# Kernel tuning notes

Measured on AMD Instinct MI355X. Metric: run time of the kernel, lower is better.

Reference implementation:

```python
import jax, jax.numpy as jnp
import numpy as np

N_EMB = 1024
HEAD_SIZE = 64
BLOCK_SIZE = 2048
B, T = 8, 2048


def setup_inputs() -> dict:
    key = jax.random.key(0)
    kx, kq, kk, kv = jax.random.split(key, 4)
    scale = 1.0 / (N_EMB ** 0.5)
    x = jax.random.normal(kx, (B, T, N_EMB), dtype=jnp.float32)
    Wq = jax.random.uniform(kq, (N_EMB, HEAD_SIZE), dtype=jnp.float32) * scale
    Wk = jax.random.uniform(kk, (N_EMB, HEAD_SIZE), dtype=jnp.float32) * scale
    Wv = jax.random.uniform(kv, (N_EMB, HEAD_SIZE), dtype=jnp.float32) * scale
    return {"x": x, "Wq": Wq, "Wk": Wk, "Wv": Wv}


def reference(x, Wq, Wk, Wv):
    # Faithful to Head.__call__ with is_training=False.
    # NOTE: original code applies NO 1/sqrt(head_size) scaling to the scores.
    Bt, Tt, _ = x.shape
    q = x @ Wq                      # (B, T, H)
    k = x @ Wk                      # (B, T, H)
    v = x @ Wv                      # (B, T, H)
    wei = jnp.einsum('bth,bsh->bts', q, k)  # (B, T, T)
    causal = jnp.tril(jnp.ones((Tt, Tt), dtype=bool))
    wei = jnp.where(causal, wei, -jnp.inf)
    wei = jax.nn.softmax(wei, axis=-1)
    out = jnp.einsum('bts,bsh->bth', wei, v)  # (B, T, H)
    return out
```

## Files before the change

### kernel.cpp

```cpp
#include <hip/hip_runtime.h>
#include <hip/hip_bf16.h>

#define BB 8
#define TT 2048
#define EE 1024
#define HH 64

typedef __attribute__((ext_vector_type(8))) short short8;
typedef __attribute__((ext_vector_type(4))) float f32x4;

__device__ inline f32x4 mfma_16x16x32(short8 a, short8 b, f32x4 c) {
  return __builtin_amdgcn_mfma_f32_16x16x32_bf16(a, b, c, 0, 0, 0);
}

__device__ inline void gload_lds16(const __hip_bfloat16* g, __hip_bfloat16* l) {
  __builtin_amdgcn_global_load_lds((const __attribute__((address_space(1))) void*)g,
                                   (__attribute__((address_space(3))) void*)l,
                                   16, 0, 0);
}

__device__ inline short f2bf(float f) {
  __hip_bfloat16 h = __float2bfloat16(f);
  return *reinterpret_cast<short*>(&h);
}
__device__ inline float bf2f(short s) {
  __hip_bfloat16 h = *reinterpret_cast<__hip_bfloat16*>(&s);
  return __bfloat162float(h);
}

__global__ void prep_w(const float* __restrict__ Wq, const float* __restrict__ Wk,
                       const float* __restrict__ Wv,
                       __hip_bfloat16* __restrict__ Wthi,
                       __hip_bfloat16* __restrict__ Wtlo) {
  const int n = blockIdx.x;
  const int m = n >> 6;
  const int h = n & 63;
  const float* W = (m == 0) ? Wq : (m == 1) ? Wk : Wv;
  const int e0 = threadIdx.x * 4;
#pragma unroll
  for (int j = 0; j < 4; ++j) {
    const float w = W[(e0 + j) * 64 + h];
    const __hip_bfloat16 hi = __float2bfloat16(w);
    Wthi[n * 1024 + e0 + j] = hi;
    Wtlo[n * 1024 + e0 + j] = __float2bfloat16(w - __bfloat162float(hi));
  }
}

__global__ __launch_bounds__(256) void qkv_gemm(
    const float* __restrict__ x,
    const __hip_bfloat16* __restrict__ Wthi, const __hip_bfloat16* __restrict__ Wtlo,
    __hip_bfloat16* __restrict__ qhi, __hip_bfloat16* __restrict__ qlo,
    __hip_bfloat16* __restrict__ khi, __hip_bfloat16* __restrict__ klo,
    __hip_bfloat16* __restrict__ vT) {
  __shared__ __hip_bfloat16 Ahi[2][64 * 72];
  __shared__ __hip_bfloat16 Alo[2][64 * 72];
  __shared__ __hip_bfloat16 Bhi[2][192 * 64];
  __shared__ __hip_bfloat16 Blo[2][128 * 64];

  const int tid  = threadIdx.x;
  const int wave = tid >> 6;
  const int lane = tid & 63;
  const int row0 = blockIdx.x * 64;

  const int lr = tid >> 2;
  const int le = (tid & 3) * 16;
  const float* xrow = x + (row0 + lr) * 1024 + le;

  f32x4 acc[12];
#pragma unroll
  for (int j = 0; j < 12; ++j) acc[j] = f32x4{0.f, 0.f, 0.f, 0.f};

  const int l15 = lane & 15, l4 = lane >> 4;

  auto issue_B = [&](int c, int buf) {
    const int g = (lane & 7) ^ ((lane >> 3) & 7);
#pragma unroll
    for (int s = 0; s < 6; ++s) {
      const int qq = wave * 6 + s;
      const int n  = qq * 8 + (lane >> 3);
      gload_lds16(Wthi + n * 1024 + c * 64 + g * 8, &Bhi[buf][qq * 512]);
      if (qq < 16)
        gload_lds16(Wtlo + n * 1024 + c * 64 + g * 8, &Blo[buf][qq * 512]);
    }
  };
  auto write_A = [&](int buf, const f32x4* xr) {
    short8 h0, h1, l0, l1;
    const float* xf = (const float*)xr;
#pragma unroll
    for (int j = 0; j < 8; ++j) {
      const float v = xf[j];
      const short h = f2bf(v);
      h0[j] = h;
      l0[j] = f2bf(v - bf2f(h));
    }
#pragma unroll
    for (int j = 0; j < 8; ++j) {
      const float v = xf[8 + j];
      const short h = f2bf(v);
      h1[j] = h;
      l1[j] = f2bf(v - bf2f(h));
    }
    *(short8*)&Ahi[buf][lr * 72 + le]     = h0;
    *(short8*)&Ahi[buf][lr * 72 + le + 8] = h1;
    *(short8*)&Alo[buf][lr * 72 + le]     = l0;
    *(short8*)&Alo[buf][lr * 72 + le + 8] = l1;
  };
  auto compute = [&](int buf) {
    const int tr = wave * 16 + l15;
    short8 ah0 = *(const short8*)&Ahi[buf][tr * 72 + l4 * 8];
    short8 ah1 = *(const short8*)&Ahi[buf][tr * 72 + 32 + l4 * 8];
    short8 al0 = *(const short8*)&Alo[buf][tr * 72 + l4 * 8];
    short8 al1 = *(const short8*)&Alo[buf][tr * 72 + 32 + l4 * 8];
#pragma unroll
    for (int j = 0; j < 12; ++j) {
      const int n  = j * 16 + l15;
      const int o0 = ((l4)     ^ (n & 7)) * 8;
      const int o1 = ((4 + l4) ^ (n & 7)) * 8;
      short8 bh0 = *(const short8*)&Bhi[buf][n * 64 + o0];
      short8 bh1 = *(const short8*)&Bhi[buf][n * 64 + o1];
      acc[j] = mfma_16x16x32(ah0, bh0, acc[j]);
      acc[j] = mfma_16x16x32(ah1, bh1, acc[j]);
      if (j < 8) {
        short8 bl0 = *(const short8*)&Blo[buf][n * 64 + o0];
        short8 bl1 = *(const short8*)&Blo[buf][n * 64 + o1];
        acc[j] = mfma_16x16x32(ah0, bl0, acc[j]);
        acc[j] = mfma_16x16x32(ah1, bl1, acc[j]);
        acc[j] = mfma_16x16x32(al0, bh0, acc[j]);
        acc[j] = mfma_16x16x32(al1, bh1, acc[j]);
      }
    }
  };

  f32x4 xr[4], xn[4];
  {
    const f32x4* p = (const f32x4*)xrow;
    xr[0] = p[0]; xr[1] = p[1]; xr[2] = p[2]; xr[3] = p[3];
  }
  issue_B(0, 0);
  __builtin_amdgcn_s_waitcnt(0);
  write_A(0, xr);
  __syncthreads();

  for (int c = 0; c < 16; ++c) {
    const int p = c & 1;
    if (c < 15) {
      const f32x4* pp = (const f32x4*)(xrow + (c + 1) * 64);
      xn[0] = pp[0]; xn[1] = pp[1]; xn[2] = pp[2]; xn[3] = pp[3];
      issue_B(c + 1, p ^ 1);
    }
    compute(p);
    if (c < 15) {
      __builtin_amdgcn_s_waitcnt(0);
      write_A(p ^ 1, xn);
    }
    __syncthreads();
  }

  const int strip = wave * 16;
#pragma unroll
  for (int j = 0; j < 12; ++j) {
    const int n  = j * 16 + l15;
    const int mm = n >> 6;
    const int h  = n & 63;
#pragma unroll
    for (int r = 0; r < 4; ++r) {
      const int trow = row0 + strip + l4 * 4 + r;
      const float val = acc[j][r];
      const __hip_bfloat16 hi = __float2bfloat16(val);
      const __hip_bfloat16 lo = __float2bfloat16(val - __bfloat162float(hi));
      if (mm == 0) {
        qhi[trow * 64 + h] = hi;
        qlo[trow * 64 + h] = lo;
      } else if (mm == 1) {
        khi[trow * 64 + h] = hi;
        klo[trow * 64 + h] = lo;
      } else {
        const int bb = trow >> 11, tl = trow & 2047;
        vT[(bb * 64 + h) * 2048 + tl] = hi;
      }
    }
  }
}

__global__ __launch_bounds__(256, 1) void attn(
    const __hip_bfloat16* __restrict__ qhi, const __hip_bfloat16* __restrict__ qlo,
    const __hip_bfloat16* __restrict__ khi, const __hip_bfloat16* __restrict__ klo,
    const __hip_bfloat16* __restrict__ vT, float* __restrict__ out) {
  __shared__ __hip_bfloat16 Psm[4][64 * 72];
  __shared__ float Osm[4][64][65];
  __shared__ float Msm[4][64];
  __shared__ float Lsm[4][64];

  const int tid   = threadIdx.x;
  const int wave  = tid >> 6;
  const int lane  = tid & 63;
  const int bid   = blockIdx.x;
  const int b     = bid & 7;
  const int strip = 31 - (bid >> 3);
  const int t0    = strip * 64;
  const int l15 = lane & 15, l4 = lane >> 4;

  const int kt_total = strip + 1;
  const int chunk    = (kt_total + 3) >> 2;
  const int ktb      = wave * chunk;
  const int kte      = min(ktb + chunk, kt_total);

  short8 qh0[4], qh1[4], ql0[4], ql1[4];
#pragma unroll
  for (int m = 0; m < 4; ++m) {
    const __hip_bfloat16* qph = qhi + (b * 2048 + t0 + m * 16 + l15) * 64;
    const __hip_bfloat16* qpl = qlo + (b * 2048 + t0 + m * 16 + l15) * 64;
    qh0[m] = *(const short8*)(qph + l4 * 8);
    qh1[m] = *(const short8*)(qph + 32 + l4 * 8);
    ql0[m] = *(const short8*)(qpl + l4 * 8);
    ql1[m] = *(const short8*)(qpl + 32 + l4 * 8);
  }

  f32x4 acc[4][4];
#pragma unroll
  for (int m = 0; m < 4; ++m)
#pragma unroll
    for (int j = 0; j < 4; ++j) acc[m][j] = f32x4{0.f, 0.f, 0.f, 0.f};
  float m_[4][4], l_[4][4];
#pragma unroll
  for (int m = 0; m < 4; ++m)
#pragma unroll
    for (int r = 0; r < 4; ++r) { m_[m][r] = -1e30f; l_[m][r] = 0.f; }

  const __hip_bfloat16* kbase_h = khi + (size_t)b * 2048 * 64;
  const __hip_bfloat16* kbase_l = klo + (size_t)b * 2048 * 64;
  const __hip_bfloat16* vbase   = vT + (size_t)b * 64 * 2048;

  for (int kt = ktb; kt < kte; ++kt) {
    const int k0 = kt << 6;
    const bool diag = (k0 == t0);

    short8 kh0[4], kh1[4], kl0[4], kl1[4];
#pragma unroll
    for (int j = 0; j < 4; ++j) {
      const __hip_bfloat16* kph = kbase_h + (k0 + j * 16 + l15) * 64;
      const __hip_bfloat16* kpl = kbase_l + (k0 + j * 16 + l15) * 64;
      kh0[j] = *(const short8*)(kph + l4 * 8);
      kh1[j] = *(const short8*)(kph + 32 + l4 * 8);
      kl0[j] = *(const short8*)(kpl + l4 * 8);
      kl1[j] = *(const short8*)(kpl + 32 + l4 * 8);
    }

#pragma unroll
    for (int m = 0; m < 4; ++m) {
      f32x4 s[4];
#pragma unroll
      for (int j = 0; j < 4; ++j) {
        if (diag && j > m) {
          s[j] = f32x4{-1e30f, -1e30f, -1e30f, -1e30f};
          continue;
        }
        f32x4 z = f32x4{0.f, 0.f, 0.f, 0.f};
        z = mfma_16x16x32(qh0[m], kh0[j], z);
        z = mfma_16x16x32(qh1[m], kh1[j], z);
        z = mfma_16x16x32(qh0[m], kl0[j], z);
        z = mfma_16x16x32(qh1[m], kl1[j], z);
        z = mfma_16x16x32(ql0[m], kh0[j], z);
        z = mfma_16x16x32(ql1[m], kh1[j], z);
        s[j] = z;
      }
      if (diag) {
#pragma unroll
        for (int j = 0; j < 4; ++j) {
          if (j != m) continue;
          const int key = j * 16 + l15;
#pragma unroll
          for (int r = 0; r < 4; ++r) {
            const int row = m * 16 + l4 * 4 + r;
            if (key > row) s[j][r] = -1e30f;
          }
        }
      }

      float mx[4], rs[4], al[4];
#pragma unroll
      for (int r = 0; r < 4; ++r)
        mx[r] = fmaxf(fmaxf(s[0][r], s[1][r]), fmaxf(s[2][r], s[3][r]));
      for (int off = 1; off < 16; off <<= 1) {
#pragma unroll
        for (int r = 0; r < 4; ++r) mx[r] = fmaxf(mx[r], __shfl_xor(mx[r], off));
      }
#pragma unroll
      for (int r = 0; r < 4; ++r) {
        const float mn = fmaxf(m_[m][r], mx[r]);
        al[r] = __expf(m_[m][r] - mn);
        m_[m][r] = mn;
        rs[r] = 0.f;
      }
#pragma unroll
      for (int j = 0; j < 4; ++j) {
#pragma unroll
        for (int r = 0; r < 4; ++r) {
          const float pv = __expf(s[j][r] - m_[m][r]);
          s[j][r] = pv;
          rs[r] += pv;
        }
      }
      for (int off = 1; off < 16; off <<= 1) {
#pragma unroll
        for (int r = 0; r < 4; ++r) rs[r] += __shfl_xor(rs[r], off);
      }
#pragma unroll
      for (int r = 0; r < 4; ++r) l_[m][r] = l_[m][r] * al[r] + rs[r];
#pragma unroll
      for (int j = 0; j < 4; ++j)
#pragma unroll
        for (int r = 0; r < 4; ++r) acc[m][j][r] *= al[r];

#pragma unroll
      for (int j = 0; j < 4; ++j)
#pragma unroll
        for (int r = 0; r < 4; ++r)
          Psm[wave][(m * 16 + l4 * 4 + r) * 72 + j * 16 + l15] =
              __float2bfloat16(s[j][r]);
    }

    short8 vf0[4], vf1[4];
#pragma unroll
    for (int j = 0; j < 4; ++j) {
      const __hip_bfloat16* vp = vbase + (j * 16 + l15) * 2048 + k0;
      vf0[j] = *(const short8*)(vp + l4 * 8);
      vf1[j] = *(const short8*)(vp + 32 + l4 * 8);
    }

    __builtin_amdgcn_s_waitcnt(0);

#pragma unroll
    for (int m = 0; m < 4; ++m) {
      short8 pf0 = *(const short8*)&Psm[wave][(m * 16 + l15) * 72 + l4 * 8];
      short8 pf1 = *(const short8*)&Psm[wave][(m * 16 + l15) * 72 + 32 + l4 * 8];
#pragma unroll
      for (int j = 0; j < 4; ++j) {
        acc[m][j] = mfma_16x16x32(pf0, vf0[j], acc[m][j]);
        acc[m][j] = mfma_16x16x32(pf1, vf1[j], acc[m][j]);
      }
    }
  }

#pragma unroll
  for (int m = 0; m < 4; ++m) {
#pragma unroll
    for (int j = 0; j < 4; ++j)
#pragma unroll
      for (int r = 0; r < 4; ++r)
        Osm[wave][m * 16 + l4 * 4 + r][j * 16 + l15] = acc[m][j][r];
    if (l15 == 0) {
#pragma unroll
      for (int r = 0; r < 4; ++r) {
        Msm[wave][m * 16 + l4 * 4 + r] = m_[m][r];
        Lsm[wave][m * 16 + l4 * 4 + r] = l_[m][r];
      }
    }
  }
  __syncthreads();

#pragma unroll
  for (int rr = 0; rr < 16; ++rr) {
    const int row = wave * 16 + rr;
    float M = fmaxf(fmaxf(Msm[0][row], Msm[1][row]),
                    fmaxf(Msm[2][row], Msm[3][row]));
    float L = 0.f, O = 0.f;
#pragma unroll
    for (int w = 0; w < 4; ++w) {
      const float a = __expf(Msm[w][row] - M);
      L += Lsm[w][row] * a;
      O += Osm[w][row][lane] * a;
    }
    out[(b * 2048 + t0 + row) * 64 + lane] = O / L;
  }
}

extern "C" void kernel_launch(void* const* d_in, const int* in_sizes, int n_in,
                              void* d_out, int out_size, void* d_ws, size_t ws_size,
                              hipStream_t stream) {
  const float* x  = (const float*)d_in[0];
  const float* Wq = (const float*)d_in[1];
  const float* Wk = (const float*)d_in[2];
  const float* Wv = (const float*)d_in[3];
  float* out = (float*)d_out;

  char* ws = (char*)d_ws;
  __hip_bfloat16* Wthi = (__hip_bfloat16*)ws;
  __hip_bfloat16* Wtlo = (__hip_bfloat16*)(ws + 393216);
  __hip_bfloat16* qhi  = (__hip_bfloat16*)(ws + 786432);
  __hip_bfloat16* qlo  = (__hip_bfloat16*)(ws + 786432 + 1 * 2097152);
  __hip_bfloat16* khi  = (__hip_bfloat16*)(ws + 786432 + 2 * 2097152);
  __hip_bfloat16* klo  = (__hip_bfloat16*)(ws + 786432 + 3 * 2097152);
  __hip_bfloat16* vT   = (__hip_bfloat16*)(ws + 786432 + 4 * 2097152);

  prep_w<<<192, 256, 0, stream>>>(Wq, Wk, Wv, Wthi, Wtlo);
  qkv_gemm<<<256, 256, 0, stream>>>(x, Wthi, Wtlo, qhi, qlo, khi, klo, vT);
  attn<<<256, 256, 0, stream>>>(qhi, qlo, khi, klo, vT, out);
}
```

Before: 172.2 us.

## Split causal attention into per-wave KV chunks with separate merge kernel

Replaces the one-block-per-strip attention kernel with a split-KV scheme. Each wave independently owns a (batch, strip, chunk) work item of up to 8 chunks, giving 1824 waves in 456 blocks at occupancy 2, and writes a normalized bf16 partial output plus max and sum to workspace. A new merge kernel combines the partials per strip. This targets the load imbalance and low occupancy of the triangular causal workload, at the cost of an extra launch, global round-trips for the partials, and bf16 rounding of partial outputs. It also narrows the waitcnt so only LDS counters are waited on.

```diff
diff --git a/kernel.cpp b/kernel.cpp
--- a/kernel.cpp
+++ b/kernel.cpp
@@ -27,6 +27,8 @@
   __hip_bfloat16 h = *reinterpret_cast<__hip_bfloat16*>(&s);
   return __bfloat162float(h);
 }
+
+#define WAIT_LGKM0() __builtin_amdgcn_s_waitcnt(0xC07F)
 
 __global__ void prep_w(const float* __restrict__ Wq, const float* __restrict__ Wk,
                        const float* __restrict__ Wv,
@@ -182,28 +184,39 @@
   }
 }
 
-__global__ __launch_bounds__(256, 1) void attn(
+__global__ __launch_bounds__(256, 2) void attn_part(
     const __hip_bfloat16* __restrict__ qhi, const __hip_bfloat16* __restrict__ qlo,
     const __hip_bfloat16* __restrict__ khi, const __hip_bfloat16* __restrict__ klo,
-    const __hip_bfloat16* __restrict__ vT, float* __restrict__ out) {
+    const __hip_bfloat16* __restrict__ vT,
+    __hip_bfloat16* __restrict__ partO, float* __restrict__ partM,
+    float* __restrict__ partL) {
   __shared__ __hip_bfloat16 Psm[4][64 * 72];
-  __shared__ float Osm[4][64][65];
-  __shared__ float Msm[4][64];
-  __shared__ float Lsm[4][64];
-
-  const int tid   = threadIdx.x;
-  const int wave  = tid >> 6;
-  const int lane  = tid & 63;
-  const int bid   = blockIdx.x;
-  const int b     = bid & 7;
-  const int strip = 31 - (bid >> 3);
-  const int t0    = strip * 64;
+
+  const int tid  = threadIdx.x;
+  const int wave = tid >> 6;
+  const int lane = tid & 63;
   const int l15 = lane & 15, l4 = lane >> 4;
 
-  const int kt_total = strip + 1;
-  const int chunk    = (kt_total + 3) >> 2;
-  const int ktb      = wave * chunk;
-  const int kte      = min(ktb + chunk, kt_total);
+  const int w = 1823 - (blockIdx.x * 4 + wave);
+  const int b = w / 228;
+  int v = w % 228;
+  int s, ci;
+  if (v < 28) {
+    s = 0;
+    while (v >= s + 1) { v -= s + 1; ++s; }
+    ci = v;
+  } else {
+    const int g = v - 28;
+    s = 7 + (g >> 3);
+    ci = g & 7;
+  }
+  const int ntile = s + 1;
+  const int nch   = (ntile < 8) ? ntile : 8;
+  const int base  = ntile / nch, rem = ntile % nch;
+  const int tb    = ci * base + ((ci < rem) ? ci : rem);
+  const int tcnt  = base + ((ci < rem) ? 1 : 0);
+  const int t0    = s * 64;
+  const int pidx  = (b * 32 + s) * 8 + ci;
 
   short8 qh0[4], qh1[4], ql0[4], ql1[4];
 #pragma unroll
@@ -231,9 +244,10 @@
   const __hip_bfloat16* kbase_l = klo + (size_t)b * 2048 * 64;
   const __hip_bfloat16* vbase   = vT + (size_t)b * 64 * 2048;
 
-  for (int kt = ktb; kt < kte; ++kt) {
+  for (int tt = 0; tt < tcnt; ++tt) {
+    const int kt = tb + tt;
     const int k0 = kt << 6;
-    const bool diag = (k0 == t0);
+    const bool diag = (kt == s);
 
     short8 kh0[4], kh1[4], kl0[4], kl1[4];
 #pragma unroll
@@ -248,11 +262,11 @@
 
 #pragma unroll
     for (int m = 0; m < 4; ++m) {
-      f32x4 s[4];
+      f32x4 s_[4];
 #pragma unroll
       for (int j = 0; j < 4; ++j) {
         if (diag && j > m) {
-          s[j] = f32x4{-1e30f, -1e30f, -1e30f, -1e30f};
+          s_[j] = f32x4{-1e30f, -1e30f, -1e30f, -1e30f};
           continue;
         }
         f32x4 z = f32x4{0.f, 0.f, 0.f, 0.f};
@@ -262,25 +276,21 @@
         z = mfma_16x16x32(qh1[m], kl1[j], z);
         z = mfma_16x16x32(ql0[m], kh0[j], z);
         z = mfma_16x16x32(ql1[m], kh1[j], z);
-        s[j] = z;
+        s_[j] = z;
       }
       if (diag) {
-#pragma unroll
-        for (int j = 0; j < 4; ++j) {
-          if (j != m) continue;
-          const int key = j * 16 + l15;
-#pragma unroll
-          for (int r = 0; r < 4; ++r) {
-            const int row = m * 16 + l4 * 4 + r;
-            if (key > row) s[j][r] = -1e30f;
-          }
+        const int key = m * 16 + l15;
+#pragma unroll
+        for (int r = 0; r < 4; ++r) {
+          const int row = m * 16 + l4 * 4 + r;
+          if (key > row) s_[m][r] = -1e30f;
         }
       }
 
       float mx[4], rs[4], al[4];
 #pragma unroll
       for (int r = 0; r < 4; ++r)
-        mx[r] = fmaxf(fmaxf(s[0][r], s[1][r]), fmaxf(s[2][r], s[3][r]));
+        mx[r] = fmaxf(fmaxf(s_[0][r], s_[1][r]), fmaxf(s_[2][r], s_[3][r]));
       for (int off = 1; off < 16; off <<= 1) {
 #pragma unroll
         for (int r = 0; r < 4; ++r) mx[r] = fmaxf(mx[r], __shfl_xor(mx[r], off));
@@ -296,8 +306,8 @@
       for (int j = 0; j < 4; ++j) {
 #pragma unroll
         for (int r = 0; r < 4; ++r) {
-          const float pv = __expf(s[j][r] - m_[m][r]);
-          s[j][r] = pv;
+          const float pv = __expf(s_[j][r] - m_[m][r]);
+          s_[j][r] = pv;
           rs[r] += pv;
         }
       }
@@ -317,7 +327,7 @@
 #pragma unroll
         for (int r = 0; r < 4; ++r)
           Psm[wave][(m * 16 + l4 * 4 + r) * 72 + j * 16 + l15] =
-              __float2bfloat16(s[j][r]);
+              __float2bfloat16(s_[j][r]);
     }
 
     short8 vf0[4], vf1[4];
@@ -328,7 +338,7 @@
       vf1[j] = *(const short8*)(vp + 32 + l4 * 8);
     }
 
-    __builtin_amdgcn_s_waitcnt(0);
+    WAIT_LGKM0();
 
 #pragma unroll
     for (int m = 0; m < 4; ++m) {
@@ -344,34 +354,49 @@
 
 #pragma unroll
   for (int m = 0; m < 4; ++m) {
+    float inv[4];
+#pragma unroll
+    for (int r = 0; r < 4; ++r) inv[r] = (l_[m][r] > 0.f) ? 1.f / l_[m][r] : 0.f;
 #pragma unroll
     for (int j = 0; j < 4; ++j)
 #pragma unroll
       for (int r = 0; r < 4; ++r)
-        Osm[wave][m * 16 + l4 * 4 + r][j * 16 + l15] = acc[m][j][r];
+        partO[(size_t)pidx * 4096 + (m * 16 + l4 * 4 + r) * 64 + j * 16 + l15] =
+            __float2bfloat16(acc[m][j][r] * inv[r]);
     if (l15 == 0) {
 #pragma unroll
       for (int r = 0; r < 4; ++r) {
-        Msm[wave][m * 16 + l4 * 4 + r] = m_[m][r];
-        Lsm[wave][m * 16 + l4 * 4 + r] = l_[m][r];
-      }
-    }
-  }
-  __syncthreads();
-
-#pragma unroll
+        partM[pidx * 64 + m * 16 + l4 * 4 + r] = m_[m][r];
+        partL[pidx * 64 + m * 16 + l4 * 4 + r] = l_[m][r];
+      }
+    }
+  }
+}
+
+__global__ __launch_bounds__(256) void attn_merge(
+    const __hip_bfloat16* __restrict__ partO, const float* __restrict__ partM,
+    const float* __restrict__ partL, float* __restrict__ out) {
+  const int bs = blockIdx.x;
+  const int b = bs >> 5, s = bs & 31;
+  const int nch = (s + 1 < 8) ? (s + 1) : 8;
+  const int tid = threadIdx.x;
+  const int h = tid & 63, rg = tid >> 6;
+
+#pragma unroll 4
   for (int rr = 0; rr < 16; ++rr) {
-    const int row = wave * 16 + rr;
-    float M = fmaxf(fmaxf(Msm[0][row], Msm[1][row]),
-                    fmaxf(Msm[2][row], Msm[3][row]));
+    const int row = rg * 16 + rr;
+    float M = -1e30f;
+    for (int c = 0; c < nch; ++c)
+      M = fmaxf(M, partM[(bs * 8 + c) * 64 + row]);
     float L = 0.f, O = 0.f;
-#pragma unroll
-    for (int w = 0; w < 4; ++w) {
-      const float a = __expf(Msm[w][row] - M);
-      L += Lsm[w][row] * a;
-      O += Osm[w][row][lane] * a;
-    }
-    out[(b * 2048 + t0 + row) * 64 + lane] = O / L;
+    for (int c = 0; c < nch; ++c) {
+      const float a = __expf(partM[(bs * 8 + c) * 64 + row] - M) *
+                      partL[(bs * 8 + c) * 64 + row];
+      L += a;
+      O += a * __bfloat162float(
+               partO[(size_t)(bs * 8 + c) * 4096 + row * 64 + h]);
+    }
+    out[(b * 2048 + s * 64 + row) * 64 + h] = O / L;
   }
 }
 
@@ -392,8 +417,13 @@
   __hip_bfloat16* khi  = (__hip_bfloat16*)(ws + 786432 + 2 * 2097152);
   __hip_bfloat16* klo  = (__hip_bfloat16*)(ws + 786432 + 3 * 2097152);
   __hip_bfloat16* vT   = (__hip_bfloat16*)(ws + 786432 + 4 * 2097152);
+  char* p = ws + 786432 + 5 * 2097152;
+  __hip_bfloat16* partO = (__hip_bfloat16*)p;
+  float* partM = (float*)(p + 16777216);
+  float* partL = (float*)(p + 16777216 + 524288);
 
   prep_w<<<192, 256, 0, stream>>>(Wq, Wk, Wv, Wthi, Wtlo);
   qkv_gemm<<<256, 256, 0, stream>>>(x, Wthi, Wtlo, qhi, qlo, khi, klo, vT);
-  attn<<<256, 256, 0, stream>>>(qhi, qlo, khi, klo, vT, out);
-}
+  attn_part<<<456, 256, 0, stream>>>(qhi, qlo, khi, klo, vT, partO, partM, partL);
+  attn_merge<<<256, 256, 0, stream>>>(partO, partM, partL, out);
+}
```

After: 252.6 us. 1.47x slower.

## Halve attention query strip to 32 rows, double grid, interleave key tiles across waves

Applied to the files above, without the earlier changes.

The attention kernel now handles 32 query rows per block instead of 64, launching 512 blocks. Waves take key tiles round-robin rather than in contiguous chunks, and launch bounds allow two blocks per CU. Register and LDS use per block drop, and the full-wait is narrowed to an LDS-only waitcnt. The aim is better load balance for the causal triangle and more occupancy. In exchange, K/V tiles are reloaded twice as often across blocks, and a diagonal tile of 64 keys is now half-masked for 32-row strips.

```diff
diff --git a/kernel.cpp b/kernel.cpp
--- a/kernel.cpp
+++ b/kernel.cpp
@@ -27,6 +27,8 @@
   __hip_bfloat16 h = *reinterpret_cast<__hip_bfloat16*>(&s);
   return __bfloat162float(h);
 }
+
+#define WAIT_LGKM0() __builtin_amdgcn_s_waitcnt(0xC07F)
 
 __global__ void prep_w(const float* __restrict__ Wq, const float* __restrict__ Wk,
                        const float* __restrict__ Wv,
@@ -182,32 +184,28 @@
   }
 }
 
-__global__ __launch_bounds__(256, 1) void attn(
+__global__ __launch_bounds__(256, 2) void attn(
     const __hip_bfloat16* __restrict__ qhi, const __hip_bfloat16* __restrict__ qlo,
     const __hip_bfloat16* __restrict__ khi, const __hip_bfloat16* __restrict__ klo,
     const __hip_bfloat16* __restrict__ vT, float* __restrict__ out) {
-  __shared__ __hip_bfloat16 Psm[4][64 * 72];
-  __shared__ float Osm[4][64][65];
-  __shared__ float Msm[4][64];
-  __shared__ float Lsm[4][64];
-
-  const int tid   = threadIdx.x;
-  const int wave  = tid >> 6;
-  const int lane  = tid & 63;
-  const int bid   = blockIdx.x;
-  const int b     = bid & 7;
-  const int strip = 31 - (bid >> 3);
-  const int t0    = strip * 64;
+  __shared__ __hip_bfloat16 Psm[4][2][16 * 72];
+  __shared__ float Osm[4][32][65];
+  __shared__ float Msm[4][32];
+  __shared__ float Lsm[4][32];
+
+  const int tid  = threadIdx.x;
+  const int wave = tid >> 6;
+  const int lane = tid & 63;
   const int l15 = lane & 15, l4 = lane >> 4;
 
-  const int kt_total = strip + 1;
-  const int chunk    = (kt_total + 3) >> 2;
-  const int ktb      = wave * chunk;
-  const int kte      = min(ktb + chunk, kt_total);
-
-  short8 qh0[4], qh1[4], ql0[4], ql1[4];
-#pragma unroll
-  for (int m = 0; m < 4; ++m) {
+  const int b  = blockIdx.x & 7;
+  const int ss = 63 - (blockIdx.x >> 3);
+  const int t0 = ss * 32;
+  const int ntiles = (ss >> 1) + 1;
+
+  short8 qh0[2], qh1[2], ql0[2], ql1[2];
+#pragma unroll
+  for (int m = 0; m < 2; ++m) {
     const __hip_bfloat16* qph = qhi + (b * 2048 + t0 + m * 16 + l15) * 64;
     const __hip_bfloat16* qpl = qlo + (b * 2048 + t0 + m * 16 + l15) * 64;
     qh0[m] = *(const short8*)(qph + l4 * 8);
@@ -216,14 +214,14 @@
     ql1[m] = *(const short8*)(qpl + 32 + l4 * 8);
   }
 
-  f32x4 acc[4][4];
-#pragma unroll
-  for (int m = 0; m < 4; ++m)
+  f32x4 acc[2][4];
+#pragma unroll
+  for (int m = 0; m < 2; ++m)
 #pragma unroll
     for (int j = 0; j < 4; ++j) acc[m][j] = f32x4{0.f, 0.f, 0.f, 0.f};
-  float m_[4][4], l_[4][4];
-#pragma unroll
-  for (int m = 0; m < 4; ++m)
+  float m_[2][4], l_[2][4];
+#pragma unroll
+  for (int m = 0; m < 2; ++m)
 #pragma unroll
     for (int r = 0; r < 4; ++r) { m_[m][r] = -1e30f; l_[m][r] = 0.f; }
 
@@ -231,9 +229,9 @@
   const __hip_bfloat16* kbase_l = klo + (size_t)b * 2048 * 64;
   const __hip_bfloat16* vbase   = vT + (size_t)b * 64 * 2048;
 
-  for (int kt = ktb; kt < kte; ++kt) {
+  for (int kt = wave; kt < ntiles; kt += 4) {
     const int k0 = kt << 6;
-    const bool diag = (k0 == t0);
+    const bool diag = (kt == ntiles - 1);
 
     short8 kh0[4], kh1[4], kl0[4], kl1[4];
 #pragma unroll
@@ -247,12 +245,13 @@
     }
 
 #pragma unroll
-    for (int m = 0; m < 4; ++m) {
-      f32x4 s[4];
+    for (int m = 0; m < 2; ++m) {
+      const int rowbase = t0 + m * 16;
+      f32x4 s_[4];
 #pragma unroll
       for (int j = 0; j < 4; ++j) {
-        if (diag && j > m) {
-          s[j] = f32x4{-1e30f, -1e30f, -1e30f, -1e30f};
+        if (diag && (k0 + j * 16) > (rowbase + 15)) {
+          s_[j] = f32x4{-1e30f, -1e30f, -1e30f, -1e30f};
           continue;
         }
         f32x4 z = f32x4{0.f, 0.f, 0.f, 0.f};
@@ -262,17 +261,16 @@
         z = mfma_16x16x32(qh1[m], kl1[j], z);
         z = mfma_16x16x32(ql0[m], kh0[j], z);
         z = mfma_16x16x32(ql1[m], kh1[j], z);
-        s[j] = z;
+        s_[j] = z;
       }
       if (diag) {
 #pragma unroll
         for (int j = 0; j < 4; ++j) {
-          if (j != m) continue;
-          const int key = j * 16 + l15;
+          const int key = k0 + j * 16 + l15;
 #pragma unroll
           for (int r = 0; r < 4; ++r) {
-            const int row = m * 16 + l4 * 4 + r;
-            if (key > row) s[j][r] = -1e30f;
+            const int row = rowbase + l4 * 4 + r;
+            if (key > row) s_[j][r] = -1e30f;
           }
         }
       }
@@ -280,7 +278,7 @@
       float mx[4], rs[4], al[4];
 #pragma unroll
       for (int r = 0; r < 4; ++r)
-        mx[r] = fmaxf(fmaxf(s[0][r], s[1][r]), fmaxf(s[2][r], s[3][r]));
+        mx[r] = fmaxf(fmaxf(s_[0][r], s_[1][r]), fmaxf(s_[2][r], s_[3][r]));
       for (int off = 1; off < 16; off <<= 1) {
 #pragma unroll
         for (int r = 0; r < 4; ++r) mx[r] = fmaxf(mx[r], __shfl_xor(mx[r], off));
@@ -296,8 +294,8 @@
       for (int j = 0; j < 4; ++j) {
 #pragma unroll
         for (int r = 0; r < 4; ++r) {
-          const float pv = __expf(s[j][r] - m_[m][r]);
-          s[j][r] = pv;
+          const float pv = __expf(s_[j][r] - m_[m][r]);
+          s_[j][r] = pv;
           rs[r] += pv;
         }
       }
@@ -316,8 +314,8 @@
       for (int j = 0; j < 4; ++j)
 #pragma unroll
         for (int r = 0; r < 4; ++r)
-          Psm[wave][(m * 16 + l4 * 4 + r) * 72 + j * 16 + l15] =
-              __float2bfloat16(s[j][r]);
+          Psm[wave][m][(l4 * 4 + r) * 72 + j * 16 + l15] =
+              __float2bfloat16(s_[j][r]);
     }
 
     short8 vf0[4], vf1[4];
@@ -328,12 +326,12 @@
       vf1[j] = *(const short8*)(vp + 32 + l4 * 8);
     }
 
-    __builtin_amdgcn_s_waitcnt(0);
-
-#pragma unroll
-    for (int m = 0; m < 4; ++m) {
-      short8 pf0 = *(const short8*)&Psm[wave][(m * 16 + l15) * 72 + l4 * 8];
-      short8 pf1 = *(const short8*)&Psm[wave][(m * 16 + l15) * 72 + 32 + l4 * 8];
+    WAIT_LGKM0();
+
+#pragma unroll
+    for (int m = 0; m < 2; ++m) {
+      short8 pf0 = *(const short8*)&Psm[wave][m][l15 * 72 + l4 * 8];
+      short8 pf1 = *(const short8*)&Psm[wave][m][l15 * 72 + 32 + l4 * 8];
 #pragma unroll
       for (int j = 0; j < 4; ++j) {
         acc[m][j] = mfma_16x16x32(pf0, vf0[j], acc[m][j]);
@@ -343,7 +341,7 @@
   }
 
 #pragma unroll
-  for (int m = 0; m < 4; ++m) {
+  for (int m = 0; m < 2; ++m) {
 #pragma unroll
     for (int j = 0; j < 4; ++j)
 #pragma unroll
@@ -360,16 +358,16 @@
   __syncthreads();
 
 #pragma unroll
-  for (int rr = 0; rr < 16; ++rr) {
-    const int row = wave * 16 + rr;
+  for (int rr = 0; rr < 8; ++rr) {
+    const int row = wave * 8 + rr;
     float M = fmaxf(fmaxf(Msm[0][row], Msm[1][row]),
                     fmaxf(Msm[2][row], Msm[3][row]));
     float L = 0.f, O = 0.f;
 #pragma unroll
-    for (int w = 0; w < 4; ++w) {
-      const float a = __expf(Msm[w][row] - M);
-      L += Lsm[w][row] * a;
-      O += Osm[w][row][lane] * a;
+    for (int w2 = 0; w2 < 4; ++w2) {
+      const float a = __expf(Msm[w2][row] - M);
+      L += a * Lsm[w2][row];
+      O += a * Osm[w2][row][lane];
     }
     out[(b * 2048 + t0 + row) * 64 + lane] = O / L;
   }
@@ -395,5 +393,5 @@
 
   prep_w<<<192, 256, 0, stream>>>(Wq, Wk, Wv, Wthi, Wtlo);
   qkv_gemm<<<256, 256, 0, stream>>>(x, Wthi, Wtlo, qhi, qlo, khi, klo, vT);
-  attn<<<256, 256, 0, stream>>>(qhi, qlo, khi, klo, vT, out);
-}
+  attn<<<512, 256, 0, stream>>>(qhi, qlo, khi, klo, vT, out);
+}
```

New measurement: 159.6 us. 7.3% less time.
